# Performance work log

Measured on AMD Instinct MI355X. Metric: run time of the kernel, lower is better.

Reference implementation:

```python
import jax, jax.numpy as jnp
import numpy as np

B, S, D, H = 4, 2048, 1024, 16
DH = D // H
NEG = -1.0e9


def setup_inputs() -> dict:
    key = jax.random.key(0)
    ks = jax.random.split(key, 12)
    sc = 1.0 / np.sqrt(D)
    inp = {
        'q': jax.random.normal(ks[0], (B, S, D), jnp.float32),
        'k': jax.random.normal(ks[1], (B, S, D), jnp.float32),
        'v': jax.random.normal(ks[2], (B, S, D), jnp.float32),
        # causal mask: 1.0 where attention is disallowed (strictly upper triangular)
        'mask': jnp.triu(jnp.ones((S, S), jnp.float32), k=1)[None, None, :, :],
        'Wq': jax.random.normal(ks[3], (D, D), jnp.float32) * sc,
        'bq': jnp.zeros((D,), jnp.float32),
        'Wk': jax.random.normal(ks[4], (D, D), jnp.float32) * sc,
        'bk': jnp.zeros((D,), jnp.float32),
        'Wv': jax.random.normal(ks[5], (D, D), jnp.float32) * sc,
        'bv': jnp.zeros((D,), jnp.float32),
        'Wo': jax.random.normal(ks[6], (D, D), jnp.float32) * sc,
        'bo': jnp.zeros((D,), jnp.float32),
    }
    return inp


def _split_heads(x):
    # [B,S,D] -> [B,H,S,DH]
    return x.reshape(B, S, H, DH).transpose(0, 2, 1, 3)


def reference(q, k, v, mask, Wq, bq, Wk, bk, Wv, bv, Wo, bo):
    _q = _split_heads(q @ Wq.T + bq)
    _k = _split_heads(k @ Wk.T + bk)
    _v = _split_heads(v @ Wv.T + bv)
    # faithful quirk: mask*-1e9 added BEFORE scaling, scale = sqrt(model_dim)
    score = jnp.einsum('bhqd,bhkd->bhqk', _q, _k) + mask * NEG
    attn = jax.nn.softmax(score / jnp.sqrt(jnp.float32(D)), axis=-1)
    ctx = jnp.einsum('bhqk,bhkd->bhqd', attn, _v)
    ctx = ctx.transpose(0, 2, 1, 3).reshape(B, S, D)
    return ctx @ Wo.T + bo
```

## Files before the change

kernel.cpp:

```cpp
#include <hip/hip_runtime.h>
#include <hip/hip_bf16.h>

#define S_ 2048
#define DH_ 64
#define NE_ 8388608

using f32x4  = __attribute__((ext_vector_type(4))) float;
using bf16x8 = __attribute__((ext_vector_type(8))) __bf16;
using bf16x4 = __attribute__((ext_vector_type(4))) __bf16;

__device__ __forceinline__ unsigned int f2bf(float f) {
    union { float f; unsigned int u; } x; x.f = f;
    return (x.u + 0x7FFFu + ((x.u >> 16) & 1u)) >> 16;
}

__device__ __forceinline__ void gl_lds16(const unsigned short* g, unsigned short* l) {
    __builtin_amdgcn_global_load_lds(
        (const __attribute__((address_space(1))) unsigned int*)(const void*)g,
        (__attribute__((address_space(3))) unsigned int*)(void*)l,
        16, 0, 0);
}

__global__ __launch_bounds__(256) void cvt_w4(const float* __restrict__ w0, const float* __restrict__ w1,
                                              const float* __restrict__ w2, const float* __restrict__ w3,
                                              unsigned short* __restrict__ out) {
    const float* src = blockIdx.y == 0 ? w0 : blockIdx.y == 1 ? w1 : blockIdx.y == 2 ? w2 : w3;
    unsigned short* dst = out + (size_t)blockIdx.y * 1048576;
    int i = (blockIdx.x * 256 + threadIdx.x) * 4;
    float4 v = *(const float4*)&src[i];
    ushort4 h;
    h.x = f2bf(v.x); h.y = f2bf(v.y); h.z = f2bf(v.z); h.w = f2bf(v.w);
    *(ushort4*)&dst[i] = h;
}

__global__ __launch_bounds__(256) void cvt_a3(const float* __restrict__ a0, const float* __restrict__ a1,
                                              const float* __restrict__ a2, unsigned short* __restrict__ out) {
    const float* src = blockIdx.y == 0 ? a0 : blockIdx.y == 1 ? a1 : a2;
    unsigned short* dst = out + (size_t)blockIdx.y * NE_;
    int i = (blockIdx.x * 256 + threadIdx.x) * 4;
    float4 v = *(const float4*)&src[i];
    ushort4 h;
    h.x = f2bf(v.x); h.y = f2bf(v.y); h.z = f2bf(v.z); h.w = f2bf(v.w);
    *(ushort4*)&dst[i] = h;
}

__global__ __launch_bounds__(512, 2) void gemm_qkv8(const unsigned short* __restrict__ actb,
                                                    const unsigned short* __restrict__ Wcat,
                                                    const float* __restrict__ bq,
                                                    const float* __restrict__ bk,
                                                    const float* __restrict__ bvv,
                                                    unsigned short* __restrict__ Qp,
                                                    unsigned short* __restrict__ Kp,
                                                    unsigned short* __restrict__ VTp,
                                                    float scq)
{
    __shared__ unsigned short lds[65536];
    unsigned short* ldsA = lds;
    unsigned short* ldsB = lds + 32768;

    const int orig = blockIdx.x;
    const int lid = (orig & 7) * 48 + (orig >> 3);
    const int bx = lid & 31;
    const int by = lid >> 5;
    const int range = by >> 2;
    const unsigned short* Aact = actb + (size_t)range * NE_;

    const int tid = threadIdx.x, lane = tid & 63, wid = tid >> 6;
    const int fr = lane & 15, fg = lane >> 4;
    const int wid_m = wid >> 2, wid_n = wid & 3;

    const int srcRow0 = wid * 16 + (lane >> 3);
    const int scolS = ((lane & 7) ^ ((lane >> 3) & 7)) << 3;

    auto STG = [&](int ldsRegion, const unsigned short* g, int grow, int kk) {
        const unsigned short* s0 = g + (size_t)(grow + srcRow0) * 1024 + kk + scolS;
        gl_lds16(s0, lds + ldsRegion + wid * 1024 + lane * 8);
        gl_lds16(s0 + 8 * 1024, lds + ldsRegion + wid * 1024 + 512 + lane * 8);
    };

    const int fx = fr & 7;
    const int vA0 = wid_m * 8192 + fr * 64 + ((fg ^ fx) << 3);
    const int vA1 = wid_m * 8192 + fr * 64 + (((4 | fg) ^ fx) << 3);
    const int vBr = (wid_n & 1) * 4096 + (wid_n >> 1) * 8192 + fr * 64;
    const int vB0 = vBr + ((fg ^ fx) << 3);
    const int vB1 = vBr + (((4 | fg) ^ fx) << 3);

    f32x4 acc[8][4] = {};
    bf16x8 bfr[4][2];

    STG(0,          Aact, bx * 256,       0);
    STG(8192,       Aact, bx * 256 + 128, 0);
    STG(32768,      Wcat, by * 256,       0);
    STG(32768+8192, Wcat, by * 256 + 128, 0);
    STG(32768+16384,       Wcat, by * 256,       64);
    STG(32768+16384+8192,  Wcat, by * 256 + 128,  64);
    asm volatile("s_waitcnt vmcnt(4)" ::: "memory");
    __builtin_amdgcn_s_barrier();

#define KTILE(BUF, ABUF, TA, BBUF, TB)                                              \
  {                                                                                 \
    _Pragma("unroll")                                                               \
    for (int q = 0; q < 4; ++q) {                                                   \
      if (q == 0) {                                                                 \
        _Pragma("unroll")                                                           \
        for (int j = 0; j < 4; ++j) {                                               \
          bfr[j][0] = *(const bf16x8*)&ldsB[(BUF)*16384 + vB0 + j*1024];            \
          bfr[j][1] = *(const bf16x8*)&ldsB[(BUF)*16384 + vB1 + j*1024];            \
        }                                                                           \
      }                                                                             \
      bf16x8 af[2][2];                                                              \
      _Pragma("unroll")                                                             \
      for (int i2 = 0; i2 < 2; ++i2) {                                              \
        af[i2][0] = *(const bf16x8*)&ldsA[(BUF)*16384 + vA0 + (q*2+i2)*1024];       \
        af[i2][1] = *(const bf16x8*)&ldsA[(BUF)*16384 + vA1 + (q*2+i2)*1024];       \
      }                                                                             \
      if (q == 0) STG((ABUF)*16384,        Aact, bx*256,       ((TA)&15)*64);       \
      if (q == 1) STG((ABUF)*16384 + 8192, Aact, bx*256 + 128, ((TA)&15)*64);       \
      if (q == 2) STG(32768 + (BBUF)*16384,        Wcat, by*256,       ((TB)&15)*64); \
      if (q == 3) { STG(32768 + (BBUF)*16384 + 8192, Wcat, by*256 + 128, ((TB)&15)*64); \
                    asm volatile("s_waitcnt vmcnt(4)" ::: "memory"); }              \
      __builtin_amdgcn_s_barrier();                                                 \
      asm volatile("s_waitcnt lgkmcnt(0)" ::: "memory");                            \
      __builtin_amdgcn_s_setprio(1);                                                \
      _Pragma("unroll")                                                             \
      for (int i2 = 0; i2 < 2; ++i2)                                                \
        _Pragma("unroll")                                                           \
        for (int j = 0; j < 4; ++j) {                                               \
          acc[q*2+i2][j] = __builtin_amdgcn_mfma_f32_16x16x32_bf16(af[i2][0], bfr[j][0], acc[q*2+i2][j], 0, 0, 0); \
          acc[q*2+i2][j] = __builtin_amdgcn_mfma_f32_16x16x32_bf16(af[i2][1], bfr[j][1], acc[q*2+i2][j], 0, 0, 0); \
        }                                                                           \
      __builtin_amdgcn_s_setprio(0);                                                \
      __builtin_amdgcn_s_barrier();                                                 \
    }                                                                               \
  }

    for (int it = 0; it < 8; ++it) {
        const int t0 = 2 * it;
        KTILE(0, 1, t0 + 1, 0, t0 + 2);
        KTILE(1, 0, t0 + 2, 1, t0 + 3);
    }
#undef KTILE

    asm volatile("s_waitcnt vmcnt(0)" ::: "memory");

    const float* bp = range == 0 ? bq : range == 1 ? bk : bvv;
    const float os = range == 0 ? scq : 1.0f;
    unsigned short* OP = range == 0 ? Qp : Kp;
    const int row00 = bx * 256 + wid_m * 128;
    const int col0r = (by & 3) * 256 + wid_n * 64;

    #pragma unroll
    for (int i = 0; i < 8; ++i) {
        #pragma unroll
        for (int j = 0; j < 4; ++j) {
            int colr = col0r + j * 16 + fr;
            float bias = bp[colr];
            int h = colr >> 6, dh = colr & 63;
            if (range == 2) {
                int row = row00 + i * 16 + fg * 4;
                int b = row >> 11, s = row & 2047;
                unsigned int w0 = f2bf(acc[i][j][0] + bias) | (f2bf(acc[i][j][1] + bias) << 16);
                unsigned int w1 = f2bf(acc[i][j][2] + bias) | (f2bf(acc[i][j][3] + bias) << 16);
                *(uint2*)&VTp[((size_t)((b << 4) + h) * 64 + dh) * 2048 + s] = make_uint2(w0, w1);
            } else {
                #pragma unroll
                for (int r = 0; r < 4; ++r) {
                    int row = row00 + i * 16 + fg * 4 + r;
                    int b = row >> 11, s = row & 2047;
                    OP[((((b << 4) + h) * 2048 + s) << 6) + dh] =
                        (unsigned short)f2bf((acc[i][j][r] + bias) * os);
                }
            }
        }
    }
}

__global__ __launch_bounds__(256) void gemm_o(const unsigned short* __restrict__ A,
                                              const unsigned short* __restrict__ Bw,
                                              const float* __restrict__ bias,
                                              float* __restrict__ Cf)
{
    constexpr int K = 1024, BK = 32, N = 1024;
    __shared__ unsigned short As[128 * BK];
    __shared__ unsigned short Bs[128 * BK];

    const int tid = threadIdx.x, lane = tid & 63, wid = tid >> 6;
    const int row0 = blockIdx.x * 128, col0 = blockIdx.y * 128;
    const int wm = (wid >> 1) * 64, wn = (wid & 1) * 64;
    const int fr = lane & 15, fg = lane >> 4;

    f32x4 acc[4][4] = {};

    const int srow = wid * 16 + (lane >> 2);
    const int scol = (lane & 3) * 8;
    const size_t abase = (size_t)(row0 + srow) * K + scol;
    const size_t bbase = (size_t)(col0 + srow) * K + scol;
    unsigned short* lA0 = &As[srow * BK + scol];
    unsigned short* lA1 = &As[(srow + 64) * BK + scol];
    unsigned short* lB0 = &Bs[srow * BK + scol];
    unsigned short* lB1 = &Bs[(srow + 64) * BK + scol];

    for (int k0 = 0; k0 < K; k0 += BK) {
        gl_lds16(&A[abase + k0], lA0);
        gl_lds16(&A[abase + (size_t)64 * K + k0], lA1);
        gl_lds16(&Bw[bbase + k0], lB0);
        gl_lds16(&Bw[bbase + (size_t)64 * K + k0], lB1);
        __syncthreads();

        bf16x8 af[4], bfr[4];
        #pragma unroll
        for (int i = 0; i < 4; ++i) af[i] = *(const bf16x8*)&As[(wm + i * 16 + fr) * BK + fg * 8];
        #pragma unroll
        for (int i = 0; i < 4; ++i) bfr[i] = *(const bf16x8*)&Bs[(wn + i * 16 + fr) * BK + fg * 8];
        #pragma unroll
        for (int i = 0; i < 4; ++i)
            #pragma unroll
            for (int j = 0; j < 4; ++j)
                acc[i][j] = __builtin_amdgcn_mfma_f32_16x16x32_bf16(af[i], bfr[j], acc[i][j], 0, 0, 0);
        __syncthreads();
    }

    #pragma unroll
    for (int i = 0; i < 4; ++i) {
        #pragma unroll
        for (int j = 0; j < 4; ++j) {
            int col = col0 + wn + j * 16 + fr;
            float bv = bias[col];
            #pragma unroll
            for (int r = 0; r < 4; ++r) {
                int row = row0 + wm + i * 16 + fg * 4 + r;
                Cf[(size_t)row * N + col] = acc[i][j][r] + bv;
            }
        }
    }
}

__global__ __launch_bounds__(512, 4) void attn_fwd5(const unsigned short* __restrict__ Qp,
                                                    const unsigned short* __restrict__ Kp,
                                                    const unsigned short* __restrict__ VTg,
                                                    unsigned short* __restrict__ ctx)
{
    __shared__ unsigned short Ks[64][68];
    __shared__ unsigned short Vt[64][68];
    __shared__ unsigned short Ps[8][16][68];

    const int lin = blockIdx.x;
    const int xcd = lin & 7;
    const int w = lin >> 3;
    const int bh = xcd * 8 + (w & 7);
    const int j = 15 - (w >> 3);
    const int b = bh >> 4, h = bh & 15;
    const int tid = threadIdx.x, lane = tid & 63, wid = tid >> 6;
    const int fr = lane & 15, fg = lane >> 4;

    const unsigned short* Qh  = Qp  + (size_t)bh * (S_ * DH_);
    const unsigned short* Kh  = Kp  + (size_t)bh * (S_ * DH_);
    const unsigned short* VTh = VTg + (size_t)bh * (DH_ * S_);

    const int srow = tid >> 3;
    const int scol = (tid & 7) * 8;

    bf16x8 ones;
    #pragma unroll
    for (int i = 0; i < 8; ++i) ones[i] = (__bf16)1.0f;

    const int q0 = j * 128;
    const int ntiles = 2 * (j + 1);
    const int rbase = q0 + wid * 16;
    const int qg = rbase + fr;

    bf16x8 qf[2];
    #pragma unroll
    for (int ks = 0; ks < 2; ++ks)
        qf[ks] = *(const bf16x8*)&Qh[(size_t)qg * 64 + ks * 32 + 8 * fg];

    f32x4 oacc[4] = {};
    float m_run = -3.0e38f, l_run = 0.0f;

    int4 kreg = *(const int4*)&Kh[(size_t)srow * 64 + scol];
    int4 vreg = *(const int4*)&VTh[(size_t)srow * 2048 + scol];

    for (int kt = 0; kt < ntiles; ++kt) {
        const int kv0 = kt * 64;
        __syncthreads();
        *(int4*)&Ks[srow][scol] = kreg;
        *(int4*)&Vt[srow][scol] = vreg;
        if (kt + 1 < ntiles) {
            const int kv1 = kv0 + 64;
            kreg = *(const int4*)&Kh[(size_t)(kv1 + srow) * 64 + scol];
            vreg = *(const int4*)&VTh[(size_t)srow * 2048 + kv1 + scol];
        }
        __syncthreads();

        if (kv0 > rbase + 15) continue;

        f32x4 sacc[4] = {};
        #pragma unroll
        for (int nt = 0; nt < 4; ++nt)
            #pragma unroll
            for (int ks = 0; ks < 2; ++ks) {
                bf16x8 kf = *(const bf16x8*)&Ks[nt * 16 + fr][ks * 32 + 8 * fg];
                sacc[nt] = __builtin_amdgcn_mfma_f32_16x16x32_bf16(kf, qf[ks], sacc[nt], 0, 0, 0);
            }

        if (kv0 + 63 > rbase) {
            const int kbase = kv0 + fg * 4;
            #pragma unroll
            for (int nt = 0; nt < 4; ++nt)
                #pragma unroll
                for (int r = 0; r < 4; ++r)
                    if (kbase + nt * 16 + r > qg) sacc[nt][r] = -3.0e38f;
        }

        float vm = sacc[0][0];
        #pragma unroll
        for (int nt = 0; nt < 4; ++nt)
            #pragma unroll
            for (int r = 0; r < 4; ++r) vm = fmaxf(vm, sacc[nt][r]);
        vm = fmaxf(vm, __shfl_xor(vm, 16));
        vm = fmaxf(vm, __shfl_xor(vm, 32));

        if (!__all(vm - m_run <= 8.0f)) {
            const float mn = fmaxf(m_run, vm);
            const float alpha = exp2f(m_run - mn);
            m_run = mn;
            l_run *= alpha;
            #pragma unroll
            for (int dt = 0; dt < 4; ++dt)
                #pragma unroll
                for (int r = 0; r < 4; ++r) oacc[dt][r] *= alpha;
        }

        #pragma unroll
        for (int nt = 0; nt < 4; ++nt) {
            bf16x4 t;
            t[0] = (__bf16)exp2f(sacc[nt][0] - m_run);
            t[1] = (__bf16)exp2f(sacc[nt][1] - m_run);
            t[2] = (__bf16)exp2f(sacc[nt][2] - m_run);
            t[3] = (__bf16)exp2f(sacc[nt][3] - m_run);
            *(bf16x4*)&Ps[wid][fr][nt * 16 + fg * 4] = t;
        }
        asm volatile("s_waitcnt lgkmcnt(0)" ::: "memory");

        bf16x8 pb[2];
        #pragma unroll
        for (int ks = 0; ks < 2; ++ks)
            pb[ks] = *(const bf16x8*)&Ps[wid][fr][ks * 32 + 8 * fg];

        f32x4 racc = {};
        #pragma unroll
        for (int ks = 0; ks < 2; ++ks)
            racc = __builtin_amdgcn_mfma_f32_16x16x32_bf16(ones, pb[ks], racc, 0, 0, 0);
        #pragma unroll
        for (int dt = 0; dt < 4; ++dt)
            #pragma unroll
            for (int ks = 0; ks < 2; ++ks) {
                bf16x8 vf = *(const bf16x8*)&Vt[dt * 16 + fr][ks * 32 + 8 * fg];
                oacc[dt] = __builtin_amdgcn_mfma_f32_16x16x32_bf16(vf, pb[ks], oacc[dt], 0, 0, 0);
            }
        l_run += racc[0];
    }

    const float linv = 1.0f / l_run;
    unsigned short* cb = &ctx[(size_t)(b * 2048 + qg) * 1024 + h * 64];
    #pragma unroll
    for (int dt = 0; dt < 4; ++dt) {
        unsigned int w0 = f2bf(oacc[dt][0] * linv) | (f2bf(oacc[dt][1] * linv) << 16);
        unsigned int w1 = f2bf(oacc[dt][2] * linv) | (f2bf(oacc[dt][3] * linv) << 16);
        *(uint2*)&cb[dt * 16 + fg * 4] = make_uint2(w0, w1);
    }
}

extern "C" void kernel_launch(void* const* d_in, const int* in_sizes, int n_in,
                              void* d_out, int out_size, void* d_ws, size_t ws_size,
                              hipStream_t stream)
{
    const float* q  = (const float*)d_in[0];
    const float* k  = (const float*)d_in[1];
    const float* v  = (const float*)d_in[2];
    const float* Wq = (const float*)d_in[4];
    const float* bq = (const float*)d_in[5];
    const float* Wk = (const float*)d_in[6];
    const float* bk = (const float*)d_in[7];
    const float* Wv = (const float*)d_in[8];
    const float* bv = (const float*)d_in[9];
    const float* Wo = (const float*)d_in[10];
    const float* bo = (const float*)d_in[11];
    float* out = (float*)d_out;

    unsigned short* Wcat = (unsigned short*)d_ws;
    unsigned short* actb = Wcat + 4 * 1048576;
    unsigned short* Qp   = actb + 3 * (size_t)NE_;
    unsigned short* Kp   = Qp + NE_;
    unsigned short* VTp  = Kp + NE_;
    unsigned short* Ctx  = VTp + NE_;

    const float SCQ = 0.045084220027780106f;

    dim3 blk(256);
    cvt_w4<<<dim3(1024, 4), blk, 0, stream>>>(Wq, Wk, Wv, Wo, Wcat);
    cvt_a3<<<dim3(8192, 3), blk, 0, stream>>>(q, k, v, actb);

    gemm_qkv8<<<dim3(384), dim3(512), 0, stream>>>(actb, Wcat, bq, bk, bv, Qp, Kp, VTp, SCQ);

    attn_fwd5<<<dim3(1024), dim3(512), 0, stream>>>(Qp, Kp, VTp, Ctx);

    gemm_o<<<dim3(64, 8), blk, 0, stream>>>(Ctx, Wcat + 3 * 1048576, bo, out);
}
```

Before: 201.3 us.

## Pair causal query tiles per block and give each wave two query rows

The attention kernel now runs 512 blocks of 4 waves instead of 1024 blocks of 8. Each block processes two 128-row query tiles, j and 15-j, so every block does the same amount of causal work. Each wave now handles 32 query rows as two 16-row MFMA groups, so every K/V fragment read from LDS feeds twice as many MFMAs. The cost is more registers per wave, fewer waves per block to hide latency, and more iterations wasted on waves that skip fully masked tiles.

```diff
diff --git a/kernel.cpp b/kernel.cpp
--- a/kernel.cpp
+++ b/kernel.cpp
@@ -235,20 +235,20 @@
     }
 }
 
-__global__ __launch_bounds__(512, 4) void attn_fwd5(const unsigned short* __restrict__ Qp,
+__global__ __launch_bounds__(256, 4) void attn_fwd6(const unsigned short* __restrict__ Qp,
                                                     const unsigned short* __restrict__ Kp,
                                                     const unsigned short* __restrict__ VTg,
                                                     unsigned short* __restrict__ ctx)
 {
     __shared__ unsigned short Ks[64][68];
     __shared__ unsigned short Vt[64][68];
-    __shared__ unsigned short Ps[8][16][68];
+    __shared__ unsigned short Ps[4][32][68];
 
     const int lin = blockIdx.x;
     const int xcd = lin & 7;
     const int w = lin >> 3;
     const int bh = xcd * 8 + (w & 7);
-    const int j = 15 - (w >> 3);
+    const int pi = w >> 3;
     const int b = bh >> 4, h = bh & 15;
     const int tid = threadIdx.x, lane = tid & 63, wid = tid >> 6;
     const int fr = lane & 15, fg = lane >> 4;
@@ -257,117 +257,157 @@
     const unsigned short* Kh  = Kp  + (size_t)bh * (S_ * DH_);
     const unsigned short* VTh = VTg + (size_t)bh * (DH_ * S_);
 
-    const int srow = tid >> 3;
-    const int scol = (tid & 7) * 8;
+    const int srow = tid >> 2;
+    const int scol = (tid & 3) * 16;
 
     bf16x8 ones;
     #pragma unroll
     for (int i = 0; i < 8; ++i) ones[i] = (__bf16)1.0f;
 
-    const int q0 = j * 128;
-    const int ntiles = 2 * (j + 1);
-    const int rbase = q0 + wid * 16;
-    const int qg = rbase + fr;
-
-    bf16x8 qf[2];
-    #pragma unroll
-    for (int ks = 0; ks < 2; ++ks)
-        qf[ks] = *(const bf16x8*)&Qh[(size_t)qg * 64 + ks * 32 + 8 * fg];
-
-    f32x4 oacc[4] = {};
-    float m_run = -3.0e38f, l_run = 0.0f;
-
-    int4 kreg = *(const int4*)&Kh[(size_t)srow * 64 + scol];
-    int4 vreg = *(const int4*)&VTh[(size_t)srow * 2048 + scol];
-
-    for (int kt = 0; kt < ntiles; ++kt) {
-        const int kv0 = kt * 64;
-        __syncthreads();
-        *(int4*)&Ks[srow][scol] = kreg;
-        *(int4*)&Vt[srow][scol] = vreg;
-        if (kt + 1 < ntiles) {
-            const int kv1 = kv0 + 64;
-            kreg = *(const int4*)&Kh[(size_t)(kv1 + srow) * 64 + scol];
-            vreg = *(const int4*)&VTh[(size_t)srow * 2048 + kv1 + scol];
+    for (int half = 0; half < 2; ++half) {
+        const int j = half ? (15 - pi) : pi;
+        const int q0 = j * 128;
+        const int ntiles = 2 * (j + 1);
+        const int rbase = q0 + wid * 32;
+
+        bf16x8 qf[2][2];
+        #pragma unroll
+        for (int m = 0; m < 2; ++m)
+            #pragma unroll
+            for (int ks = 0; ks < 2; ++ks)
+                qf[m][ks] = *(const bf16x8*)&Qh[(size_t)(rbase + m * 16 + fr) * 64 + ks * 32 + 8 * fg];
+
+        f32x4 oacc[2][4] = {};
+        float m_run[2] = {-3.0e38f, -3.0e38f}, l_run[2] = {0.0f, 0.0f};
+
+        int4 kreg[2], vreg[2];
+        #pragma unroll
+        for (int u = 0; u < 2; ++u) {
+            kreg[u] = *(const int4*)&Kh[(size_t)srow * 64 + scol + 8 * u];
+            vreg[u] = *(const int4*)&VTh[(size_t)srow * 2048 + scol + 8 * u];
         }
-        __syncthreads();
-
-        if (kv0 > rbase + 15) continue;
-
-        f32x4 sacc[4] = {};
-        #pragma unroll
-        for (int nt = 0; nt < 4; ++nt)
-            #pragma unroll
-            for (int ks = 0; ks < 2; ++ks) {
-                bf16x8 kf = *(const bf16x8*)&Ks[nt * 16 + fr][ks * 32 + 8 * fg];
-                sacc[nt] = __builtin_amdgcn_mfma_f32_16x16x32_bf16(kf, qf[ks], sacc[nt], 0, 0, 0);
-            }
-
-        if (kv0 + 63 > rbase) {
-            const int kbase = kv0 + fg * 4;
+
+        for (int kt = 0; kt < ntiles; ++kt) {
+            const int kv0 = kt * 64;
+            __syncthreads();
+            #pragma unroll
+            for (int u = 0; u < 2; ++u) {
+                *(int4*)&Ks[srow][scol + 8 * u] = kreg[u];
+                *(int4*)&Vt[srow][scol + 8 * u] = vreg[u];
+            }
+            if (kt + 1 < ntiles) {
+                const int kv1 = kv0 + 64;
+                #pragma unroll
+                for (int u = 0; u < 2; ++u) {
+                    kreg[u] = *(const int4*)&Kh[(size_t)(kv1 + srow) * 64 + scol + 8 * u];
+                    vreg[u] = *(const int4*)&VTh[(size_t)srow * 2048 + kv1 + scol + 8 * u];
+                }
+            }
+            __syncthreads();
+
+            if (kv0 > rbase + 31) continue;
+
+            f32x4 sacc[2][4] = {};
             #pragma unroll
             for (int nt = 0; nt < 4; ++nt)
                 #pragma unroll
-                for (int r = 0; r < 4; ++r)
-                    if (kbase + nt * 16 + r > qg) sacc[nt][r] = -3.0e38f;
+                for (int ks = 0; ks < 2; ++ks) {
+                    bf16x8 kf = *(const bf16x8*)&Ks[nt * 16 + fr][ks * 32 + 8 * fg];
+                    sacc[0][nt] = __builtin_amdgcn_mfma_f32_16x16x32_bf16(kf, qf[0][ks], sacc[0][nt], 0, 0, 0);
+                    sacc[1][nt] = __builtin_amdgcn_mfma_f32_16x16x32_bf16(kf, qf[1][ks], sacc[1][nt], 0, 0, 0);
+                }
+
+            #pragma unroll
+            for (int m = 0; m < 2; ++m) {
+                const int qg = rbase + m * 16 + fr;
+                if (kv0 + 63 > rbase + m * 16) {
+                    const int kbase = kv0 + fg * 4;
+                    #pragma unroll
+                    for (int nt = 0; nt < 4; ++nt)
+                        #pragma unroll
+                        for (int r = 0; r < 4; ++r)
+                            if (kbase + nt * 16 + r > qg) sacc[m][nt][r] = -3.0e38f;
+                }
+            }
+
+            float vm[2];
+            #pragma unroll
+            for (int m = 0; m < 2; ++m) {
+                float v = sacc[m][0][0];
+                #pragma unroll
+                for (int nt = 0; nt < 4; ++nt)
+                    #pragma unroll
+                    for (int r = 0; r < 4; ++r) v = fmaxf(v, sacc[m][nt][r]);
+                v = fmaxf(v, __shfl_xor(v, 16));
+                v = fmaxf(v, __shfl_xor(v, 32));
+                vm[m] = v;
+            }
+
+            if (!__all(vm[0] - m_run[0] <= 8.0f && vm[1] - m_run[1] <= 8.0f)) {
+                #pragma unroll
+                for (int m = 0; m < 2; ++m) {
+                    const float mn = fmaxf(m_run[m], vm[m]);
+                    const float alpha = exp2f(m_run[m] - mn);
+                    m_run[m] = mn;
+                    l_run[m] *= alpha;
+                    #pragma unroll
+                    for (int dt = 0; dt < 4; ++dt)
+                        #pragma unroll
+                        for (int r = 0; r < 4; ++r) oacc[m][dt][r] *= alpha;
+                }
+            }
+
+            #pragma unroll
+            for (int m = 0; m < 2; ++m)
+                #pragma unroll
+                for (int nt = 0; nt < 4; ++nt) {
+                    bf16x4 t;
+                    t[0] = (__bf16)exp2f(sacc[m][nt][0] - m_run[m]);
+                    t[1] = (__bf16)exp2f(sacc[m][nt][1] - m_run[m]);
+                    t[2] = (__bf16)exp2f(sacc[m][nt][2] - m_run[m]);
+                    t[3] = (__bf16)exp2f(sacc[m][nt][3] - m_run[m]);
+                    *(bf16x4*)&Ps[wid][m * 16 + fr][nt * 16 + fg * 4] = t;
+                }
+            asm volatile("s_waitcnt lgkmcnt(0)" ::: "memory");
+
+            bf16x8 pb[2][2];
+            #pragma unroll
+            for (int m = 0; m < 2; ++m)
+                #pragma unroll
+                for (int ks = 0; ks < 2; ++ks)
+                    pb[m][ks] = *(const bf16x8*)&Ps[wid][m * 16 + fr][ks * 32 + 8 * fg];
+
+            f32x4 racc[2] = {};
+            #pragma unroll
+            for (int m = 0; m < 2; ++m)
+                #pragma unroll
+                for (int ks = 0; ks < 2; ++ks)
+                    racc[m] = __builtin_amdgcn_mfma_f32_16x16x32_bf16(ones, pb[m][ks], racc[m], 0, 0, 0);
+
+            #pragma unroll
+            for (int dt = 0; dt < 4; ++dt)
+                #pragma unroll
+                for (int ks = 0; ks < 2; ++ks) {
+                    bf16x8 vf = *(const bf16x8*)&Vt[dt * 16 + fr][ks * 32 + 8 * fg];
+                    oacc[0][dt] = __builtin_amdgcn_mfma_f32_16x16x32_bf16(vf, pb[0][ks], oacc[0][dt], 0, 0, 0);
+                    oacc[1][dt] = __builtin_amdgcn_mfma_f32_16x16x32_bf16(vf, pb[1][ks], oacc[1][dt], 0, 0, 0);
+                }
+            l_run[0] += racc[0][0];
+            l_run[1] += racc[1][0];
         }
 
-        float vm = sacc[0][0];
-        #pragma unroll
-        for (int nt = 0; nt < 4; ++nt)
-            #pragma unroll
-            for (int r = 0; r < 4; ++r) vm = fmaxf(vm, sacc[nt][r]);
-        vm = fmaxf(vm, __shfl_xor(vm, 16));
-        vm = fmaxf(vm, __shfl_xor(vm, 32));
-
-        if (!__all(vm - m_run <= 8.0f)) {
-            const float mn = fmaxf(m_run, vm);
-            const float alpha = exp2f(m_run - mn);
-            m_run = mn;
-            l_run *= alpha;
-            #pragma unroll
-            for (int dt = 0; dt < 4; ++dt)
-                #pragma unroll
-                for (int r = 0; r < 4; ++r) oacc[dt][r] *= alpha;
+        #pragma unroll
+        for (int m = 0; m < 2; ++m) {
+            const float linv = 1.0f / l_run[m];
+            const int qg = rbase + m * 16 + fr;
+            unsigned short* cb = &ctx[(size_t)(b * 2048 + qg) * 1024 + h * 64];
+            #pragma unroll
+            for (int dt = 0; dt < 4; ++dt) {
+                unsigned int w0 = f2bf(oacc[m][dt][0] * linv) | (f2bf(oacc[m][dt][1] * linv) << 16);
+                unsigned int w1 = f2bf(oacc[m][dt][2] * linv) | (f2bf(oacc[m][dt][3] * linv) << 16);
+                *(uint2*)&cb[dt * 16 + fg * 4] = make_uint2(w0, w1);
+            }
         }
-
-        #pragma unroll
-        for (int nt = 0; nt < 4; ++nt) {
-            bf16x4 t;
-            t[0] = (__bf16)exp2f(sacc[nt][0] - m_run);
-            t[1] = (__bf16)exp2f(sacc[nt][1] - m_run);
-            t[2] = (__bf16)exp2f(sacc[nt][2] - m_run);
-            t[3] = (__bf16)exp2f(sacc[nt][3] - m_run);
-            *(bf16x4*)&Ps[wid][fr][nt * 16 + fg * 4] = t;
-        }
-        asm volatile("s_waitcnt lgkmcnt(0)" ::: "memory");
-
-        bf16x8 pb[2];
-        #pragma unroll
-        for (int ks = 0; ks < 2; ++ks)
-            pb[ks] = *(const bf16x8*)&Ps[wid][fr][ks * 32 + 8 * fg];
-
-        f32x4 racc = {};
-        #pragma unroll
-        for (int ks = 0; ks < 2; ++ks)
-            racc = __builtin_amdgcn_mfma_f32_16x16x32_bf16(ones, pb[ks], racc, 0, 0, 0);
-        #pragma unroll
-        for (int dt = 0; dt < 4; ++dt)
-            #pragma unroll
-            for (int ks = 0; ks < 2; ++ks) {
-                bf16x8 vf = *(const bf16x8*)&Vt[dt * 16 + fr][ks * 32 + 8 * fg];
-                oacc[dt] = __builtin_amdgcn_mfma_f32_16x16x32_bf16(vf, pb[ks], oacc[dt], 0, 0, 0);
-            }
-        l_run += racc[0];
-    }
-
-    const float linv = 1.0f / l_run;
-    unsigned short* cb = &ctx[(size_t)(b * 2048 + qg) * 1024 + h * 64];
-    #pragma unroll
-    for (int dt = 0; dt < 4; ++dt) {
-        unsigned int w0 = f2bf(oacc[dt][0] * linv) | (f2bf(oacc[dt][1] * linv) << 16);
-        unsigned int w1 = f2bf(oacc[dt][2] * linv) | (f2bf(oacc[dt][3] * linv) << 16);
-        *(uint2*)&cb[dt * 16 + fg * 4] = make_uint2(w0, w1);
     }
 }
 
@@ -403,7 +443,7 @@
 
     gemm_qkv8<<<dim3(384), dim3(512), 0, stream>>>(actb, Wcat, bq, bk, bv, Qp, Kp, VTp, SCQ);
 
-    attn_fwd5<<<dim3(1024), dim3(512), 0, stream>>>(Qp, Kp, VTp, Ctx);
+    attn_fwd6<<<dim3(512), dim3(256), 0, stream>>>(Qp, Kp, VTp, Ctx);
 
     gemm_o<<<dim3(64, 8), blk, 0, stream>>>(Ctx, Wcat + 3 * 1048576, bo, out);
 }
```

Result: slower. 233.2 us (+15.8%).

## Split attention into 64-row query tiles with 4-wave blocks

Applied to the files above, without the earlier changes.

The attention kernel now uses 2048 blocks of 256 threads, each covering 64 query rows, instead of 1024 blocks of 512 threads covering 128 rows. Each thread stages two 16-byte chunks of K and V^T per tile rather than one. Smaller blocks with finer causal granularity should balance the triangular work better and raise occupancy. In exchange, each K/V tile is loaded from global memory by twice as many blocks, doubling that load traffic.

```diff
diff --git a/kernel.cpp b/kernel.cpp
--- a/kernel.cpp
+++ b/kernel.cpp
@@ -235,20 +235,20 @@
     }
 }
 
-__global__ __launch_bounds__(512, 4) void attn_fwd5(const unsigned short* __restrict__ Qp,
+__global__ __launch_bounds__(256, 6) void attn_fwd8(const unsigned short* __restrict__ Qp,
                                                     const unsigned short* __restrict__ Kp,
                                                     const unsigned short* __restrict__ VTg,
                                                     unsigned short* __restrict__ ctx)
 {
     __shared__ unsigned short Ks[64][68];
     __shared__ unsigned short Vt[64][68];
-    __shared__ unsigned short Ps[8][16][68];
+    __shared__ unsigned short Ps[4][16][68];
 
     const int lin = blockIdx.x;
     const int xcd = lin & 7;
     const int w = lin >> 3;
     const int bh = xcd * 8 + (w & 7);
-    const int j = 15 - (w >> 3);
+    const int p = 31 - (w >> 3);
     const int b = bh >> 4, h = bh & 15;
     const int tid = threadIdx.x, lane = tid & 63, wid = tid >> 6;
     const int fr = lane & 15, fg = lane >> 4;
@@ -257,15 +257,15 @@
     const unsigned short* Kh  = Kp  + (size_t)bh * (S_ * DH_);
     const unsigned short* VTh = VTg + (size_t)bh * (DH_ * S_);
 
-    const int srow = tid >> 3;
-    const int scol = (tid & 7) * 8;
+    const int srow = tid >> 2;
+    const int scol = (tid & 3) * 16;
 
     bf16x8 ones;
     #pragma unroll
     for (int i = 0; i < 8; ++i) ones[i] = (__bf16)1.0f;
 
-    const int q0 = j * 128;
-    const int ntiles = 2 * (j + 1);
+    const int q0 = p * 64;
+    const int ntiles = p + 1;
     const int rbase = q0 + wid * 16;
     const int qg = rbase + fr;
 
@@ -277,18 +277,28 @@
     f32x4 oacc[4] = {};
     float m_run = -3.0e38f, l_run = 0.0f;
 
-    int4 kreg = *(const int4*)&Kh[(size_t)srow * 64 + scol];
-    int4 vreg = *(const int4*)&VTh[(size_t)srow * 2048 + scol];
+    int4 kreg[2], vreg[2];
+    #pragma unroll
+    for (int u = 0; u < 2; ++u) {
+        kreg[u] = *(const int4*)&Kh[(size_t)srow * 64 + scol + 8 * u];
+        vreg[u] = *(const int4*)&VTh[(size_t)srow * 2048 + scol + 8 * u];
+    }
 
     for (int kt = 0; kt < ntiles; ++kt) {
         const int kv0 = kt * 64;
         __syncthreads();
-        *(int4*)&Ks[srow][scol] = kreg;
-        *(int4*)&Vt[srow][scol] = vreg;
+        #pragma unroll
+        for (int u = 0; u < 2; ++u) {
+            *(int4*)&Ks[srow][scol + 8 * u] = kreg[u];
+            *(int4*)&Vt[srow][scol + 8 * u] = vreg[u];
+        }
         if (kt + 1 < ntiles) {
             const int kv1 = kv0 + 64;
-            kreg = *(const int4*)&Kh[(size_t)(kv1 + srow) * 64 + scol];
-            vreg = *(const int4*)&VTh[(size_t)srow * 2048 + kv1 + scol];
+            #pragma unroll
+            for (int u = 0; u < 2; ++u) {
+                kreg[u] = *(const int4*)&Kh[(size_t)(kv1 + srow) * 64 + scol + 8 * u];
+                vreg[u] = *(const int4*)&VTh[(size_t)srow * 2048 + kv1 + scol + 8 * u];
+            }
         }
         __syncthreads();
 
@@ -403,7 +413,7 @@
 
     gemm_qkv8<<<dim3(384), dim3(512), 0, stream>>>(actb, Wcat, bq, bk, bv, Qp, Kp, VTp, SCQ);
 
-    attn_fwd5<<<dim3(1024), dim3(512), 0, stream>>>(Qp, Kp, VTp, Ctx);
+    attn_fwd8<<<dim3(2048), dim3(256), 0, stream>>>(Qp, Kp, VTp, Ctx);
 
     gemm_o<<<dim3(64, 8), blk, 0, stream>>>(Ctx, Wcat + 3 * 1048576, bo, out);
 }
```

New measurement: 286.8 us. 42.4% more time.
